# Kernel optimization log

Measured on AMD Instinct MI355X. Metric: run time of the kernel, lower is better.

Reference implementation:

```python
import jax, jax.numpy as jnp
import numpy as np

N_NODES = 50000
N_EDGES = 1600000
DIM = 512


def setup_inputs() -> dict:
    key = jax.random.key(0)
    k1, k2, k3, k4, k5 = jax.random.split(key, 5)
    x = jax.random.normal(k1, (N_NODES, DIM), dtype=jnp.float32)
    adj_rows = jax.random.randint(k2, (N_EDGES,), 0, N_NODES, dtype=jnp.int32)
    adj_cols = jax.random.randint(k3, (N_EDGES,), 0, N_NODES, dtype=jnp.int32)
    adj_vals = jax.random.uniform(k4, (N_EDGES,), dtype=jnp.float32)
    # fc1 weight [out_dim, in_dim], kaiming-normal-ish init
    weight = jax.random.normal(k5, (DIM, DIM), dtype=jnp.float32) * np.float32(np.sqrt(2.0 / DIM))
    scale = jnp.full((1,), 1.5, dtype=jnp.float32)
    return {"x": x, "adj_rows": adj_rows, "adj_cols": adj_cols,
            "adj_vals": adj_vals, "weight": weight, "scale": scale}


def reference(x, adj_rows, adj_cols, adj_vals, weight, scale):
    # dropout in eval mode -> identity
    N, D = x.shape
    # dense linear: y = x @ W^T
    y = jnp.einsum('nd,od->no', x, weight)
    # sparse adj @ y  (COO SpMM via gather + segment_sum)
    y = jax.ops.segment_sum(adj_vals[:, None] * y[adj_cols], adj_rows,
                            num_segments=N)
    # sp_norm: mean-center over nodes, scale by global RMS^{-1} * (1+scale) * sqrt(D)
    y_t = y - jnp.mean(y, axis=0, keepdims=True)
    y_norm = jnp.mean(jnp.sum(y_t * y_t, axis=1)) ** -0.5
    y = y_t * y_norm * (1.0 + scale) * jnp.float32(np.sqrt(D))
    # activation (relu), then residual (input_dim == output_dim)
    y = jax.nn.relu(y)
    return y + x
```

## Files before the change

### kernel.cpp

```cpp
#include <hip/hip_runtime.h>
#include <hip/hip_bf16.h>
#include <cstdint>
#include <cstddef>

#define N_NODES 50000
#define DIM 512
#define N_EDGES 1600000
#define NT 25
#define NB (N_NODES * NT)

typedef __bf16 bf16;
typedef __bf16 bf16x8 __attribute__((ext_vector_type(8)));
typedef __bf16 bf16x4 __attribute__((ext_vector_type(4)));
typedef float floatx4 __attribute__((ext_vector_type(4)));

__global__ void cast_kernel(const float* __restrict__ in, bf16* __restrict__ out, int n4) {
    int i = blockIdx.x * blockDim.x + threadIdx.x;
    if (i >= n4) return;
    float4 v = reinterpret_cast<const float4*>(in)[i];
    bf16x4 o;
    o[0] = (bf16)v.x; o[1] = (bf16)v.y; o[2] = (bf16)v.z; o[3] = (bf16)v.w;
    reinterpret_cast<bf16x4*>(out)[i] = o;
}

__global__ void hist_kernel(const int* __restrict__ rows, const int* __restrict__ cols,
                            int* __restrict__ cnt, int E) {
    int i = blockIdx.x * blockDim.x + threadIdx.x;
    if (i < E) {
        int key = rows[i] * NT + (cols[i] >> 11);
        atomicAdd(&cnt[key], 1);
    }
}

__global__ __launch_bounds__(1024) void scanA_kernel(const int* __restrict__ cnt,
                                                     int* __restrict__ row_start,
                                                     int* __restrict__ blksum, int n) {
    __shared__ int s[1024];
    const int t = threadIdx.x;
    int i = blockIdx.x * 1024 + t;
    int v = (i < n) ? cnt[i] : 0;
    s[t] = v;
    __syncthreads();
    for (int off = 1; off < 1024; off <<= 1) {
        int u = (t >= off) ? s[t - off] : 0;
        __syncthreads();
        s[t] += u;
        __syncthreads();
    }
    if (i < n) row_start[i] = s[t] - v;
    if (t == 1023) blksum[blockIdx.x] = s[1023];
}

__global__ __launch_bounds__(1024) void scanB_kernel(const int* __restrict__ blksum,
                                                     int* __restrict__ blkoff, int nb) {
    __shared__ int s[1024];
    const int t = threadIdx.x;
    const int base = t * 2;
    int a = (base < nb) ? blksum[base] : 0;
    int b = (base + 1 < nb) ? blksum[base + 1] : 0;
    s[t] = a + b;
    __syncthreads();
    for (int off = 1; off < 1024; off <<= 1) {
        int u = (t >= off) ? s[t - off] : 0;
        __syncthreads();
        s[t] += u;
        __syncthreads();
    }
    int excl = (t == 0) ? 0 : s[t - 1];
    if (base < nb) blkoff[base] = excl;
    if (base + 1 < nb) blkoff[base + 1] = excl + a;
}

__global__ __launch_bounds__(1024) void scanC_kernel(int* __restrict__ row_start,
                                                     const int* __restrict__ blkoff,
                                                     int* __restrict__ cursor, int n) {
    int i = blockIdx.x * 1024 + threadIdx.x;
    if (i >= n) return;
    int v = row_start[i] + blkoff[i >> 10];
    row_start[i] = v;
    cursor[i] = v;
    if (i == n - 1) row_start[n] = N_EDGES;
}

__global__ void scatter_kernel(const int* __restrict__ rows, const int* __restrict__ cols,
                               const float* __restrict__ vals, int* __restrict__ cursor,
                               int2* __restrict__ ecv, int E) {
    int i = blockIdx.x * blockDim.x + threadIdx.x;
    if (i >= E) return;
    int c = cols[i];
    int key = rows[i] * NT + (c >> 11);
    int p = atomicAdd(&cursor[key], 1);
    ecv[p] = make_int2(c, __float_as_int(vals[i]));
}

__global__ __launch_bounds__(256) void gemm_kernel(const bf16* __restrict__ A,
                                                   const bf16* __restrict__ B,
                                                   bf16* __restrict__ C) {
    __shared__ bf16 lA[128 * 32];
    __shared__ bf16 lB[128 * 32];
    const int t = threadIdx.x;
    const int wave = t >> 6;
    const int lane = t & 63;
    const int rowBase = blockIdx.x * 128;
    const int colBase = blockIdx.y * 128;
    const int wm = (wave >> 1) * 64;
    const int wn = (wave & 1) * 64;
    floatx4 acc[4][4] = {};

    const int r_a = t >> 2;
    const int kk = (t & 3) * 8;

    const int l15 = lane & 15;
    const int koff = (lane >> 4) * 8;

    for (int k0 = 0; k0 < DIM; k0 += 32) {
#pragma unroll
        for (int j = 0; j < 2; j++) {
            int row = rowBase + r_a + j * 64;
            if (row > N_NODES - 1) row = N_NODES - 1;
            const bf16* g = A + (size_t)row * DIM + k0 + kk;
            bf16* l = lA + wave * 512 + j * 2048;
            __builtin_amdgcn_global_load_lds(
                (const __attribute__((address_space(1))) void*)g,
                (__attribute__((address_space(3))) void*)l, 16, 0, 0);
        }
#pragma unroll
        for (int j = 0; j < 2; j++) {
            int row = colBase + r_a + j * 64;
            const bf16* g = B + (size_t)row * DIM + k0 + kk;
            bf16* l = lB + wave * 512 + j * 2048;
            __builtin_amdgcn_global_load_lds(
                (const __attribute__((address_space(1))) void*)g,
                (__attribute__((address_space(3))) void*)l, 16, 0, 0);
        }
        __syncthreads();
        bf16x8 af[4], bfr[4];
#pragma unroll
        for (int i = 0; i < 4; i++)
            af[i] = *reinterpret_cast<const bf16x8*>(lA + (wm + i * 16 + l15) * 32 + koff);
#pragma unroll
        for (int j = 0; j < 4; j++)
            bfr[j] = *reinterpret_cast<const bf16x8*>(lB + (wn + j * 16 + l15) * 32 + koff);
#pragma unroll
        for (int i = 0; i < 4; i++)
#pragma unroll
            for (int j = 0; j < 4; j++)
                acc[i][j] = __builtin_amdgcn_mfma_f32_16x16x32_bf16(af[i], bfr[j], acc[i][j], 0, 0, 0);
        __syncthreads();
    }
    const int rquad = (lane >> 4) * 4;
#pragma unroll
    for (int i = 0; i < 4; i++) {
#pragma unroll
        for (int reg = 0; reg < 4; reg++) {
            int gr = rowBase + wm + i * 16 + rquad + reg;
            if (gr >= N_NODES) continue;
#pragma unroll
            for (int j = 0; j < 4; j++) {
                int gc = colBase + wn + j * 16 + l15;
                C[(size_t)gr * DIM + gc] = (bf16)acc[i][j][reg];
            }
        }
    }
}

__device__ __forceinline__ float blo(uint32_t w) { return __uint_as_float(w << 16); }
__device__ __forceinline__ float bhi(uint32_t w) { return __uint_as_float(w & 0xffff0000u); }

__device__ __forceinline__ void fmac8(float* acc, float v, const uint4& w) {
    acc[0] += v * blo(w.x); acc[1] += v * bhi(w.x);
    acc[2] += v * blo(w.y); acc[3] += v * bhi(w.y);
    acc[4] += v * blo(w.z); acc[5] += v * bhi(w.z);
    acc[6] += v * blo(w.w); acc[7] += v * bhi(w.w);
}

__global__ __launch_bounds__(256) void spmm_kernel(const int* __restrict__ row_start,
                                                   const int2* __restrict__ ecv,
                                                   const bf16* __restrict__ y,
                                                   float* __restrict__ y2) {
    const int wave = threadIdx.x >> 6;
    const int lane = threadIdx.x & 63;
    const int r = blockIdx.x * 4 + wave;
    const int s = row_start[r * NT];
    const int e = row_start[(r + 1) * NT];
    float acc[8] = {0.f, 0.f, 0.f, 0.f, 0.f, 0.f, 0.f, 0.f};
    const uint32_t* yb = reinterpret_cast<const uint32_t*>(y);

    int i = s;
    for (; i + 3 < e; i += 4) {
        int2 e0 = ecv[i], e1 = ecv[i + 1], e2 = ecv[i + 2], e3 = ecv[i + 3];
        uint4 w0 = *reinterpret_cast<const uint4*>(yb + (size_t)e0.x * 256 + lane * 4);
        uint4 w1 = *reinterpret_cast<const uint4*>(yb + (size_t)e1.x * 256 + lane * 4);
        uint4 w2 = *reinterpret_cast<const uint4*>(yb + (size_t)e2.x * 256 + lane * 4);
        uint4 w3 = *reinterpret_cast<const uint4*>(yb + (size_t)e3.x * 256 + lane * 4);
        fmac8(acc, __int_as_float(e0.y), w0);
        fmac8(acc, __int_as_float(e1.y), w1);
        fmac8(acc, __int_as_float(e2.y), w2);
        fmac8(acc, __int_as_float(e3.y), w3);
    }
    for (; i < e; i++) {
        int2 e0 = ecv[i];
        uint4 w0 = *reinterpret_cast<const uint4*>(yb + (size_t)e0.x * 256 + lane * 4);
        fmac8(acc, __int_as_float(e0.y), w0);
    }
    float4* out = reinterpret_cast<float4*>(y2 + (size_t)r * DIM + lane * 8);
    out[0] = make_float4(acc[0], acc[1], acc[2], acc[3]);
    out[1] = make_float4(acc[4], acc[5], acc[6], acc[7]);
}

__global__ __launch_bounds__(256) void reduce_kernel(const float* __restrict__ y2,
                                                     float* __restrict__ colsum,
                                                     float* __restrict__ totsq) {
    const int t = threadIdx.x;
    const int d2 = t * 2;
    float c0 = 0.f, c1 = 0.f, sq = 0.f;
    for (int r = blockIdx.x; r < N_NODES; r += gridDim.x) {
        float2 v = *reinterpret_cast<const float2*>(y2 + (size_t)r * DIM + d2);
        c0 += v.x; c1 += v.y;
        sq += v.x * v.x + v.y * v.y;
    }
    atomicAdd(&colsum[d2], c0);
    atomicAdd(&colsum[d2 + 1], c1);
    __shared__ float ssq[256];
    ssq[t] = sq;
    __syncthreads();
    for (int off = 128; off > 0; off >>= 1) {
        if (t < off) ssq[t] += ssq[t + off];
        __syncthreads();
    }
    if (t == 0) atomicAdd(totsq, ssq[0]);
}

__global__ void scalar_kernel(const float* __restrict__ colsum, const float* __restrict__ totsq,
                              const float* __restrict__ scale, float* __restrict__ sfac) {
    __shared__ float sm[512];
    const int t = threadIdx.x;
    float mu = colsum[t] * (1.0f / N_NODES);
    sm[t] = mu * mu;
    __syncthreads();
    for (int off = 256; off > 0; off >>= 1) {
        if (t < off) sm[t] += sm[t + off];
        __syncthreads();
    }
    if (t == 0) {
        float var = totsq[0] * (1.0f / N_NODES) - sm[0];
        sfac[0] = rsqrtf(var) * (1.0f + scale[0]) * sqrtf((float)DIM);
    }
}

__global__ void final_kernel(float* __restrict__ y2, const float* __restrict__ x,
                             const float* __restrict__ colsum, const float* __restrict__ sfac,
                             int n4) {
    int i = blockIdx.x * blockDim.x + threadIdx.x;
    if (i >= n4) return;
    const float invN = 1.0f / N_NODES;
    float4 v = reinterpret_cast<float4*>(y2)[i];
    float4 xv = reinterpret_cast<const float4*>(x)[i];
    float4 mu = reinterpret_cast<const float4*>(colsum)[i & 127];
    float s = sfac[0];
    v.x = fmaxf((v.x - mu.x * invN) * s, 0.0f) + xv.x;
    v.y = fmaxf((v.y - mu.y * invN) * s, 0.0f) + xv.y;
    v.z = fmaxf((v.z - mu.z * invN) * s, 0.0f) + xv.z;
    v.w = fmaxf((v.w - mu.w * invN) * s, 0.0f) + xv.w;
    reinterpret_cast<float4*>(y2)[i] = v;
}

extern "C" void kernel_launch(void* const* d_in, const int* in_sizes, int n_in,
                              void* d_out, int out_size, void* d_ws, size_t ws_size,
                              hipStream_t stream) {
    const float* x        = (const float*)d_in[0];
    const int*   adj_rows = (const int*)d_in[1];
    const int*   adj_cols = (const int*)d_in[2];
    const float* adj_vals = (const float*)d_in[3];
    const float* weight   = (const float*)d_in[4];
    const float* scale    = (const float*)d_in[5];
    float* out = (float*)d_out;

    char* ws = (char*)d_ws;
    size_t off = 0;
    auto alloc = [&](size_t b) {
        char* p = ws + off;
        off += (b + 255) & ~(size_t)255;
        return p;
    };
    const int nblk = (NB + 1023) / 1024;
    bf16*  xb        = (bf16*)alloc((size_t)N_NODES * DIM * 2);
    int2*  ecv       = (int2*)xb;
    bf16*  Wb        = (bf16*)alloc((size_t)DIM * DIM * 2);
    bf16*  y         = (bf16*)alloc((size_t)N_NODES * DIM * 2);
    int*   cnt       = (int*)alloc((size_t)NB * 4);
    int*   cursor    = cnt;
    int*   row_start = (int*)alloc((size_t)(NB + 1) * 4);
    int*   blksum    = (int*)alloc((size_t)nblk * 4);
    int*   blkoff    = (int*)alloc((size_t)nblk * 4);
    float* colsum    = (float*)alloc(512 * 4);
    float* totsq     = (float*)alloc(4);
    float* sfac      = (float*)alloc(4);
    (void)ws_size; (void)in_sizes; (void)n_in; (void)out_size;

    hipMemsetAsync(cnt, 0, (size_t)NB * 4, stream);
    hipMemsetAsync(colsum, 0, 512 * 4, stream);
    hipMemsetAsync(totsq, 0, 4, stream);

    const int n4x = N_NODES * DIM / 4;
    const int n4w = DIM * DIM / 4;
    cast_kernel<<<(n4x + 255) / 256, 256, 0, stream>>>(x, xb, n4x);
    cast_kernel<<<(n4w + 255) / 256, 256, 0, stream>>>(weight, Wb, n4w);

    gemm_kernel<<<dim3((N_NODES + 127) / 128, DIM / 128), 256, 0, stream>>>(xb, Wb, y);

    hist_kernel<<<(N_EDGES + 255) / 256, 256, 0, stream>>>(adj_rows, adj_cols, cnt, N_EDGES);
    scanA_kernel<<<nblk, 1024, 0, stream>>>(cnt, row_start, blksum, NB);
    scanB_kernel<<<1, 1024, 0, stream>>>(blksum, blkoff, nblk);
    scanC_kernel<<<nblk, 1024, 0, stream>>>(row_start, blkoff, cursor, NB);
    scatter_kernel<<<(N_EDGES + 255) / 256, 256, 0, stream>>>(adj_rows, adj_cols, adj_vals,
                                                              cursor, ecv, N_EDGES);

    spmm_kernel<<<N_NODES / 4, 256, 0, stream>>>(row_start, ecv, y, out);

    reduce_kernel<<<256, 256, 0, stream>>>(out, colsum, totsq);
    scalar_kernel<<<1, 512, 0, stream>>>(colsum, totsq, scale, sfac);
    final_kernel<<<(n4x + 255) / 256, 256, 0, stream>>>(out, x, colsum, sfac, n4x);
}
```

Measured before the change: 750.9 us.

## Sweep SpMM over column tiles with persistent waves holding multiple rows

The SpMM now uses 4096 persistent waves, each accumulating 13 rows in registers. It iterates over the 25 column tiles in the outer loop so that every wave works on the same column band of y at the same time, which is meant to improve L2 reuse of the gathered rows. The cost is much higher register pressure from 104 accumulators per lane, serial per-edge loops with no unrolling, and possible load imbalance. The reduce kernel is also doubled to 512 blocks and processes two rows per iteration.

```diff
diff --git a/kernel.cpp b/kernel.cpp
--- a/kernel.cpp
+++ b/kernel.cpp
@@ -164,6 +164,9 @@
     }
 }
 
+#define SWEEP_WAVES 4096
+#define ROWS_PER_WAVE 13
+
 __device__ __forceinline__ float blo(uint32_t w) { return __uint_as_float(w << 16); }
 __device__ __forceinline__ float bhi(uint32_t w) { return __uint_as_float(w & 0xffff0000u); }
 
@@ -174,50 +177,67 @@
     acc[6] += v * blo(w.w); acc[7] += v * bhi(w.w);
 }
 
-__global__ __launch_bounds__(256) void spmm_kernel(const int* __restrict__ row_start,
-                                                   const int2* __restrict__ ecv,
-                                                   const bf16* __restrict__ y,
-                                                   float* __restrict__ y2) {
-    const int wave = threadIdx.x >> 6;
+__global__ __launch_bounds__(256, 4) void spmm_kernel(const int* __restrict__ row_start,
+                                                      const int2* __restrict__ ecv,
+                                                      const bf16* __restrict__ y,
+                                                      float* __restrict__ y2) {
+    const int wid = (blockIdx.x * 4) + (threadIdx.x >> 6);
     const int lane = threadIdx.x & 63;
-    const int r = blockIdx.x * 4 + wave;
-    const int s = row_start[r * NT];
-    const int e = row_start[(r + 1) * NT];
-    float acc[8] = {0.f, 0.f, 0.f, 0.f, 0.f, 0.f, 0.f, 0.f};
     const uint32_t* yb = reinterpret_cast<const uint32_t*>(y);
-
-    int i = s;
-    for (; i + 3 < e; i += 4) {
-        int2 e0 = ecv[i], e1 = ecv[i + 1], e2 = ecv[i + 2], e3 = ecv[i + 3];
-        uint4 w0 = *reinterpret_cast<const uint4*>(yb + (size_t)e0.x * 256 + lane * 4);
-        uint4 w1 = *reinterpret_cast<const uint4*>(yb + (size_t)e1.x * 256 + lane * 4);
-        uint4 w2 = *reinterpret_cast<const uint4*>(yb + (size_t)e2.x * 256 + lane * 4);
-        uint4 w3 = *reinterpret_cast<const uint4*>(yb + (size_t)e3.x * 256 + lane * 4);
-        fmac8(acc, __int_as_float(e0.y), w0);
-        fmac8(acc, __int_as_float(e1.y), w1);
-        fmac8(acc, __int_as_float(e2.y), w2);
-        fmac8(acc, __int_as_float(e3.y), w3);
-    }
-    for (; i < e; i++) {
-        int2 e0 = ecv[i];
-        uint4 w0 = *reinterpret_cast<const uint4*>(yb + (size_t)e0.x * 256 + lane * 4);
-        fmac8(acc, __int_as_float(e0.y), w0);
-    }
-    float4* out = reinterpret_cast<float4*>(y2 + (size_t)r * DIM + lane * 8);
-    out[0] = make_float4(acc[0], acc[1], acc[2], acc[3]);
-    out[1] = make_float4(acc[4], acc[5], acc[6], acc[7]);
-}
-
+    const int laneo = lane * 4;
+
+    float acc[ROWS_PER_WAVE][8];
+#pragma unroll
+    for (int k = 0; k < ROWS_PER_WAVE; k++)
+#pragma unroll
+        for (int j = 0; j < 8; j++) acc[k][j] = 0.f;
+
+    const int* rs = row_start + wid * NT;
+
+    for (int t = 0; t < NT; t++) {
+#pragma unroll
+        for (int k = 0; k < ROWS_PER_WAVE; k++) {
+            const int r = wid + k * SWEEP_WAVES;
+            if (r < N_NODES) {
+                const int* p = rs + k * (SWEEP_WAVES * NT) + t;
+                int s = p[0];
+                int e = p[1];
+                for (int i = s; i < e; i++) {
+                    int2 ed = ecv[i];
+                    uint4 w = *reinterpret_cast<const uint4*>(yb + (size_t)ed.x * 256 + laneo);
+                    fmac8(acc[k], __int_as_float(ed.y), w);
+                }
+            }
+        }
+    }
+
+#pragma unroll
+    for (int k = 0; k < ROWS_PER_WAVE; k++) {
+        const int r = wid + k * SWEEP_WAVES;
+        if (r < N_NODES) {
+            float4* out = reinterpret_cast<float4*>(y2 + (size_t)r * DIM + lane * 8);
+            out[0] = make_float4(acc[k][0], acc[k][1], acc[k][2], acc[k][3]);
+            out[1] = make_float4(acc[k][4], acc[k][5], acc[k][6], acc[k][7]);
+        }
+    }
+}
+
+#define RED_GRID 512
 __global__ __launch_bounds__(256) void reduce_kernel(const float* __restrict__ y2,
                                                      float* __restrict__ colsum,
                                                      float* __restrict__ totsq) {
     const int t = threadIdx.x;
     const int d2 = t * 2;
     float c0 = 0.f, c1 = 0.f, sq = 0.f;
-    for (int r = blockIdx.x; r < N_NODES; r += gridDim.x) {
+    for (int r = blockIdx.x; r < N_NODES; r += RED_GRID * 2) {
         float2 v = *reinterpret_cast<const float2*>(y2 + (size_t)r * DIM + d2);
-        c0 += v.x; c1 += v.y;
-        sq += v.x * v.x + v.y * v.y;
+        int r2 = r + RED_GRID;
+        float2 u = (r2 < N_NODES)
+                       ? *reinterpret_cast<const float2*>(y2 + (size_t)r2 * DIM + d2)
+                       : make_float2(0.f, 0.f);
+        c0 += v.x + u.x;
+        c1 += v.y + u.y;
+        sq += v.x * v.x + v.y * v.y + u.x * u.x + u.y * u.y;
     }
     atomicAdd(&colsum[d2], c0);
     atomicAdd(&colsum[d2 + 1], c1);
@@ -316,9 +336,9 @@
     scatter_kernel<<<(N_EDGES + 255) / 256, 256, 0, stream>>>(adj_rows, adj_cols, adj_vals,
                                                               cursor, ecv, N_EDGES);
 
-    spmm_kernel<<<N_NODES / 4, 256, 0, stream>>>(row_start, ecv, y, out);
-
-    reduce_kernel<<<256, 256, 0, stream>>>(out, colsum, totsq);
+    spmm_kernel<<<1024, 256, 0, stream>>>(row_start, ecv, y, out);
+
+    reduce_kernel<<<RED_GRID, 256, 0, stream>>>(out, colsum, totsq);
     scalar_kernel<<<1, 512, 0, stream>>>(colsum, totsq, scale, sfac);
     final_kernel<<<(n4x + 255) / 256, 256, 0, stream>>>(out, x, colsum, sfac, n4x);
 }
```

Result: slower. 872.1 us (+16.2%).
